# Kernel optimization log

Measured on AMD Instinct MI355X. Metric: run time of the kernel, lower is better.

## Reference

```python
import jax, jax.numpy as jnp
import numpy as np

NUM_REL = 5
NUM_BASES = 8
HID = 128
OUT = 64
IN_FEAT = 256
N_PER_TYPE = 50000
N_NODES = 2 * N_PER_TYPE
N_EDGES = 1000000
EPS = 1e-5  # PairNorm eps


def setup_inputs() -> dict:
    key = jax.random.key(0)
    ks = jax.random.split(key, 14)
    inp = {
        "x_author": jax.random.normal(ks[0], (N_PER_TYPE, IN_FEAT), jnp.float32),
        "x_paper": jax.random.normal(ks[1], (N_PER_TYPE, IN_FEAT), jnp.float32),
        "edge_index": jax.random.randint(ks[2], (2, N_EDGES), 0, N_NODES, jnp.int32),
        "edge_type": jax.random.randint(ks[3], (N_EDGES,), 0, NUM_REL, jnp.int32),
        # per-node-type input projections (nn.Linear)
        "proj_author_w": jax.random.normal(ks[4], (IN_FEAT, HID), jnp.float32) / np.sqrt(IN_FEAT),
        "proj_author_b": jnp.zeros((HID,), jnp.float32),
        "proj_paper_w": jax.random.normal(ks[5], (IN_FEAT, HID), jnp.float32) / np.sqrt(IN_FEAT),
        "proj_paper_b": jnp.zeros((HID,), jnp.float32),
        # RGCNConv layer 0 (hidden -> hidden), basis decomposition, root weight, no bias
        "comp0": jax.random.normal(ks[6], (NUM_REL, NUM_BASES), jnp.float32) / np.sqrt(NUM_BASES),
        "basis0": jax.random.normal(ks[7], (NUM_BASES, HID, HID), jnp.float32) / np.sqrt(HID),
        "root0": jax.random.normal(ks[8], (HID, HID), jnp.float32) / np.sqrt(HID),
        # RGCNConv layer 1 (hidden -> out)
        "comp1": jax.random.normal(ks[9], (NUM_REL, NUM_BASES), jnp.float32) / np.sqrt(NUM_BASES),
        "basis1": jax.random.normal(ks[10], (NUM_BASES, HID, OUT), jnp.float32) / np.sqrt(HID),
        "root1": jax.random.normal(ks[11], (HID, OUT), jnp.float32) / np.sqrt(HID),
    }
    return inp


def pairnorm(x):
    # PyG PairNorm (scale=1, scale_individually=False)
    x = x - x.mean(axis=0, keepdims=True)
    return x / jnp.sqrt(EPS + (x * x).sum(-1).mean())


def rgcn_conv(x, edge_index, edge_type, comp, basis, root):
    # weight[r] = sum_b comp[r,b] * basis[b]  -> [R, Fin, Fout]
    W = jnp.einsum('rb,bio->rio', comp, basis)
    src, dst = edge_index[0], edge_index[1]
    msgs = x[src]                                   # [E, Fin] gather
    seg = dst * NUM_REL + edge_type                 # per (node, relation) segment
    agg = jax.ops.segment_sum(msgs, seg, num_segments=N_NODES * NUM_REL)
    agg = agg.reshape(N_NODES, NUM_REL, -1)         # [N, R, Fin]
    cnt = jax.ops.segment_sum(jnp.ones((msgs.shape[0],), x.dtype), seg,
                              num_segments=N_NODES * NUM_REL).reshape(N_NODES, NUM_REL)
    mean = agg / jnp.maximum(cnt, 1.0)[..., None]   # mean aggregation (0 if no edges)
    return jnp.einsum('nrf,rfo->no', mean, W) + x @ root


def reference(x_author, x_paper, edge_index, edge_type,
              proj_author_w, proj_author_b, proj_paper_w, proj_paper_b,
              comp0, basis0, root0, comp1, basis1, root1):
    h_a = jax.nn.relu(x_author @ proj_author_w + proj_author_b)
    h_p = jax.nn.relu(x_paper @ proj_paper_w + proj_paper_b)
    x = jnp.concatenate([h_a, h_p], axis=0)         # [N, HID]
    x = jax.nn.relu(rgcn_conv(x, edge_index, edge_type, comp0, basis0, root0))
    x = pairnorm(x)
    x_latent = x
    x = rgcn_conv(x, edge_index, edge_type, comp1, basis1, root1)
    x = pairnorm(x)
    return (x, x_latent)
```

## Files before the change

kernel.cpp:

```cpp
#include <hip/hip_runtime.h>
#include <hip/hip_bf16.h>

constexpr int NPT    = 50000;
constexpr int NN     = 100000;
constexpr int NE     = 1000000;
constexpr int HID    = 128;
constexpr int OUTF   = 64;
constexpr int INF    = 256;
constexpr int NREL   = 5;
constexpr int NSEG   = NN * NREL;

typedef __attribute__((ext_vector_type(8))) short short8v;
typedef __attribute__((ext_vector_type(4))) float f32x4;

__device__ __forceinline__ ushort f2bf(float x) {
    uint u = __builtin_bit_cast(uint, x);
    uint r = (u + 0x7FFFu + ((u >> 16) & 1u)) >> 16;
    return (ushort)r;
}
__device__ __forceinline__ float bfhi(uint raw) {
    return __builtin_bit_cast(float, raw & 0xFFFF0000u);
}
__device__ __forceinline__ float bflo(uint raw) {
    return __builtin_bit_cast(float, raw << 16);
}

__device__ __forceinline__ void build_wbT_body(const float* __restrict__ comp,
                                               const float* __restrict__ basis,
                                               const float* __restrict__ root,
                                               ushort* __restrict__ wbT,
                                               int fout, int passOff, int idx) {
    int col = idx >> 7, k = idx & 127;
    float v;
    if (col < 320) {
        int r = col >> 6, f = (col & 63) + passOff;
        v = 0.f;
#pragma unroll
        for (int b = 0; b < 8; b++)
            v += comp[r * 8 + b] * basis[(b * 128 + k) * fout + f];
    } else {
        v = root[k * fout + (col - 320) + passOff];
    }
    wbT[col * 128 + k] = f2bf(v);
}

__global__ void prep_kernel(const float* __restrict__ comp0, const float* __restrict__ basis0,
                            const float* __restrict__ root0,
                            const float* __restrict__ comp1, const float* __restrict__ basis1,
                            const float* __restrict__ root1,
                            const float* __restrict__ paw, const float* __restrict__ ppw,
                            ushort* __restrict__ wbT0a, ushort* __restrict__ wbT0b,
                            ushort* __restrict__ wbT1,
                            ushort* __restrict__ wpa, ushort* __restrict__ wpp,
                            int* __restrict__ cnt, float* __restrict__ statscr,
                            int* __restrict__ recs_pad) {
    const int b = blockIdx.x, t = threadIdx.x;
    if (b < 1954) {
        int i = b * 256 + t;
        if (i < NSEG) cnt[i] = 0;
    } else if (b < 1979) {
        statscr[(b - 1954) * 256 + t] = 0.f;
    } else if (b == 1979) {
        if (t < 128) recs_pad[t] = 0;
    } else if (b < 2172) {
        build_wbT_body(comp0, basis0, root0, wbT0a, HID, 0, (b - 1980) * 256 + t);
    } else if (b < 2364) {
        build_wbT_body(comp0, basis0, root0, wbT0b, HID, 64, (b - 2172) * 256 + t);
    } else if (b < 2556) {
        build_wbT_body(comp1, basis1, root1, wbT1, OUTF, 0, (b - 2364) * 256 + t);
    } else if (b < 2684) {
        int i = (b - 2556) * 256 + t;
        wpa[(size_t)(i & 127) * 256 + (i >> 7)] = f2bf(paw[i]);
    } else {
        int i = (b - 2684) * 256 + t;
        wpp[(size_t)(i & 127) * 256 + (i >> 7)] = f2bf(ppw[i]);
    }
}

__launch_bounds__(256)
__global__ void proj_hist(const float* __restrict__ xa, const float* __restrict__ xp,
                          const ushort* __restrict__ wTa, const ushort* __restrict__ wTp,
                          const float* __restrict__ ba, const float* __restrict__ bp,
                          ushort* __restrict__ x0b,
                          const int* __restrict__ ei, const int* __restrict__ et,
                          int* __restrict__ cnt, int* __restrict__ rank) {
    __shared__ ushort sx[16][264];
    __shared__ ushort so[16][132];
    const int tid = threadIdx.x;
    if (blockIdx.x >= 1250) {
        int e = (blockIdx.x - 1250) * 256 + tid;
        if (e < NE) {
            int seg = ei[NE + e] * NREL + et[e];
            rank[e] = atomicAdd(&cnt[seg], 1);
        }
        return;
    }
    const bool author = blockIdx.x < 625;
    const int tile0 = (blockIdx.x - (author ? 0 : 625)) * 5;
    const float* x = author ? xa : xp;
    const ushort* wT = author ? wTa : wTp;
    const float* bias = author ? ba : bp;
    const int typeBase = author ? 0 : NPT;

    const int wave = tid >> 6, lane = tid & 63;
    const int row = lane & 15, g = lane >> 4;
    const int fcol = wave * 32 + row;

    const ushort* wp0 = wT + (size_t)fcol * 256 + g * 8;
    short8v bA[8], bB[8];
#pragma unroll
    for (int kk = 0; kk < 8; kk++) bA[kk] = *(const short8v*)&wp0[kk * 32];
#pragma unroll
    for (int kk = 0; kk < 8; kk++) bB[kk] = *(const short8v*)&wp0[16 * 256 + kk * 32];
    const float bv0 = bias[fcol], bv1 = bias[fcol + 16];

    const int sr = tid >> 4, part = tid & 15;
    const int fnode = tid >> 4, fb = (tid & 15) * 8;

    for (int t = 0; t < 5; t++) {
        const int nloc = (tile0 + t) * 16;
        {
            size_t rowoff = (size_t)(nloc + sr) * INF + part * 16;
#pragma unroll
            for (int ii = 0; ii < 4; ii++) {
                float4 v = *(const float4*)&x[rowoff + ii * 4];
                ushort4 h = {f2bf(v.x), f2bf(v.y), f2bf(v.z), f2bf(v.w)};
                *(ushort4*)&sx[sr][part * 16 + ii * 4] = h;
            }
        }
        __syncthreads();
        short8v a[8];
#pragma unroll
        for (int kk = 0; kk < 8; kk++) a[kk] = *(const short8v*)&sx[row][kk * 32 + g * 8];
        {
            f32x4 acc0 = {0.f, 0.f, 0.f, 0.f};
            f32x4 acc1 = {0.f, 0.f, 0.f, 0.f};
#pragma unroll
            for (int kk = 0; kk < 8; kk++) {
                acc0 = __builtin_amdgcn_mfma_f32_16x16x32_bf16(a[kk], bA[kk], acc0, 0, 0, 0);
                acc1 = __builtin_amdgcn_mfma_f32_16x16x32_bf16(a[kk], bB[kk], acc1, 0, 0, 0);
            }
#pragma unroll
            for (int q = 0; q < 4; q++) {
                so[g * 4 + q][fcol]      = f2bf(fmaxf(acc0[q] + bv0, 0.f));
                so[g * 4 + q][fcol + 16] = f2bf(fmaxf(acc1[q] + bv1, 0.f));
            }
        }
        __syncthreads();
        {
            ushort4 v0 = *(const ushort4*)&so[fnode][fb];
            ushort4 v1 = *(const ushort4*)&so[fnode][fb + 4];
            size_t gbase = (size_t)(typeBase + nloc + fnode) * 128 + fb;
            *(ushort4*)&x0b[gbase] = v0;
            *(ushort4*)&x0b[gbase + 4] = v1;
        }
    }
}

__global__ void scan1(const int* __restrict__ cnt, int* __restrict__ offs,
                      int* __restrict__ bsums, int n) {
    __shared__ int lds[256];
    const int t = threadIdx.x;
    const int base = blockIdx.x * 2048 + t * 8;
    int vals[8];
    int s = 0;
#pragma unroll
    for (int v = 0; v < 8; v++) {
        int idx = base + v;
        vals[v] = (idx < n) ? cnt[idx] : 0;
        s += vals[v];
    }
    lds[t] = s;
    __syncthreads();
    for (int off = 1; off < 256; off <<= 1) {
        int x = lds[t];
        int y = (t >= off) ? lds[t - off] : 0;
        __syncthreads();
        lds[t] = x + y;
        __syncthreads();
    }
    int run = (t > 0) ? lds[t - 1] : 0;
    if (t == 255) bsums[blockIdx.x] = lds[255];
#pragma unroll
    for (int v = 0; v < 8; v++) {
        int idx = base + v;
        if (idx < n) offs[idx] = run;
        run += vals[v];
    }
}

__global__ void scan2(const int* __restrict__ bsums, int* __restrict__ bsums2, int nb) {
    __shared__ int lds[256];
    const int t = threadIdx.x;
    lds[t] = (t < nb) ? bsums[t] : 0;
    __syncthreads();
    for (int off = 1; off < 256; off <<= 1) {
        int x = lds[t];
        int y = (t >= off) ? lds[t - off] : 0;
        __syncthreads();
        lds[t] = x + y;
        __syncthreads();
    }
    if (t < nb) bsums2[t] = (t > 0) ? lds[t - 1] : 0;
}

__global__ void scan3_desc(const int* __restrict__ offs, const int* __restrict__ bsums2,
                           const int* __restrict__ cnt, int2* __restrict__ desc, int n) {
    int i = blockIdx.x * blockDim.x + threadIdx.x;
    if (i < n) {
        int2 d = {offs[i] + bsums2[i >> 11], cnt[i]};
        desc[i] = d;
    }
}

__global__ void scatter_kernel(const int* __restrict__ ei, const int* __restrict__ et,
                               const int* __restrict__ rank,
                               const int2* __restrict__ desc, int2* __restrict__ recs) {
    int e = blockIdx.x * blockDim.x + threadIdx.x;
    if (e < NE) {
        int src = ei[e];
        int dst = ei[NE + e];
        int r = et[e];
        int2 d = desc[dst * NREL + r];
        int c = d.y;
        float sc = 1.f / (float)((c > 1) ? c : 1);
        int2 rec = {r * NN + src, __builtin_bit_cast(int, sc)};
        recs[d.x + rank[e]] = rec;
    }
}

__launch_bounds__(256)
__global__ void ytab_gemm0(const ushort* __restrict__ xin,
                           const ushort* __restrict__ wbT_a, const ushort* __restrict__ wbT_b,
                           ushort* __restrict__ ytab, float* __restrict__ hout) {
    __shared__ ushort sx[32][136];
    __shared__ ushort so[32][328];
    __shared__ float sroot[32][68];
    const int tid = threadIdx.x;
    const bool first = blockIdx.x < 625;
    const int tile0 = (first ? blockIdx.x : blockIdx.x - 625) * 5;
    const ushort* wbT = first ? wbT_a : wbT_b;
    const int outOff = first ? 0 : 64;
    const int wave = tid >> 6, lane = tid & 63;
    const int row = lane & 15, g = lane >> 4;
    const int wbase = wave * 96;

    const ushort* wp = wbT + (size_t)(wbase + row) * 128 + g * 8;
    short8v B[6][4];
#pragma unroll
    for (int t = 0; t < 6; t++)
#pragma unroll
        for (int kk = 0; kk < 4; kk++)
            B[t][kk] = *(const short8v*)&wp[t * 2048 + kk * 32];

    const int sr = tid >> 3, scl = (tid & 7) * 16;
    const int fnode = tid >> 3, fb = (tid & 7) * 8;

    for (int tt = 0; tt < 5; tt++) {
        const int n0 = (tile0 + tt) * 32;
        {
            const ushort* src = &xin[(size_t)(n0 + sr) * 128 + scl];
            *(short8v*)&sx[sr][scl] = *(const short8v*)&src[0];
            *(short8v*)&sx[sr][scl + 8] = *(const short8v*)&src[8];
        }
        __syncthreads();

        short8v a[2][4];
#pragma unroll
        for (int m = 0; m < 2; m++)
#pragma unroll
            for (int kk = 0; kk < 4; kk++)
                a[m][kk] = *(const short8v*)&sx[m * 16 + row][kk * 32 + g * 8];

#pragma unroll
        for (int t = 0; t < 6; t++) {
            f32x4 acc0 = {0.f, 0.f, 0.f, 0.f};
            f32x4 acc1 = {0.f, 0.f, 0.f, 0.f};
#pragma unroll
            for (int kk = 0; kk < 4; kk++) {
                acc0 = __builtin_amdgcn_mfma_f32_16x16x32_bf16(a[0][kk], B[t][kk], acc0, 0, 0, 0);
                acc1 = __builtin_amdgcn_mfma_f32_16x16x32_bf16(a[1][kk], B[t][kk], acc1, 0, 0, 0);
            }
            const int col = wbase + t * 16 + row;
            if (col < 320) {
#pragma unroll
                for (int q = 0; q < 4; q++) {
                    so[g * 4 + q][col] = f2bf(acc0[q]);
                    so[16 + g * 4 + q][col] = f2bf(acc1[q]);
                }
            } else {
                const int f = col - 320;
#pragma unroll
                for (int q = 0; q < 4; q++) {
                    sroot[g * 4 + q][f] = acc0[q];
                    sroot[16 + g * 4 + q][f] = acc1[q];
                }
            }
        }
        __syncthreads();

        {
#pragma unroll
            for (int r = 0; r < NREL; r++) {
                short8v v = *(const short8v*)&so[fnode][r * 64 + fb];
                *(short8v*)&ytab[(size_t)r * NN * 128 + (size_t)(n0 + fnode) * 128
                                 + outOff + fb] = v;
            }
            float4 r0 = *(const float4*)&sroot[fnode][fb];
            float4 r1 = *(const float4*)&sroot[fnode][fb + 4];
            float* hp = &hout[(size_t)(n0 + fnode) * HID + outOff + fb];
            *(float4*)&hp[0] = r0;
            *(float4*)&hp[4] = r1;
        }
    }
}

__launch_bounds__(256)
__global__ void ytab_gemm1(float* __restrict__ h0x, const float* __restrict__ mu,
                           const ushort* __restrict__ wbT,
                           ushort* __restrict__ ytab, float* __restrict__ h1) {
    __shared__ ushort sx[32][136];
    __shared__ ushort so[32][328];
    __shared__ float sroot[32][68];
    const int tid = threadIdx.x;
    const int tile0 = blockIdx.x * 5;
    const int wave = tid >> 6, lane = tid & 63;
    const int row = lane & 15, g = lane >> 4;
    const int wbase = wave * 96;

    const ushort* wp = wbT + (size_t)(wbase + row) * 128 + g * 8;
    short8v B[6][4];
#pragma unroll
    for (int t = 0; t < 6; t++)
#pragma unroll
        for (int kk = 0; kk < 4; kk++)
            B[t][kk] = *(const short8v*)&wp[t * 2048 + kk * 32];

    const int sr = tid >> 3, scl = (tid & 7) * 16;
    const int fnode = tid >> 3, fb = (tid & 7) * 8;

    float m[16];
#pragma unroll
    for (int i = 0; i < 16; i++) m[i] = mu[scl + i];
    const float s = mu[128];

    for (int tt = 0; tt < 5; tt++) {
        const int n0 = (tile0 + tt) * 32;
        {
            float* hp = &h0x[(size_t)(n0 + sr) * 128 + scl];
            float v[16];
#pragma unroll
            for (int i = 0; i < 4; i++) {
                float4 t4 = *(const float4*)&hp[i * 4];
                v[i * 4 + 0] = (t4.x - m[i * 4 + 0]) * s;
                v[i * 4 + 1] = (t4.y - m[i * 4 + 1]) * s;
                v[i * 4 + 2] = (t4.z - m[i * 4 + 2]) * s;
                v[i * 4 + 3] = (t4.w - m[i * 4 + 3]) * s;
            }
            ushort hb[16];
#pragma unroll
            for (int i = 0; i < 16; i++) hb[i] = f2bf(v[i]);
#pragma unroll
            for (int i = 0; i < 4; i++) {
                float4 t4 = {v[i * 4], v[i * 4 + 1], v[i * 4 + 2], v[i * 4 + 3]};
                *(float4*)&hp[i * 4] = t4;
            }
            *(short8v*)&sx[sr][scl] = *(const short8v*)&hb[0];
            *(short8v*)&sx[sr][scl + 8] = *(const short8v*)&hb[8];
        }
        __syncthreads();

        short8v a[2][4];
#pragma unroll
        for (int mi = 0; mi < 2; mi++)
#pragma unroll
            for (int kk = 0; kk < 4; kk++)
                a[mi][kk] = *(const short8v*)&sx[mi * 16 + row][kk * 32 + g * 8];

#pragma unroll
        for (int t = 0; t < 6; t++) {
            f32x4 acc0 = {0.f, 0.f, 0.f, 0.f};
            f32x4 acc1 = {0.f, 0.f, 0.f, 0.f};
#pragma unroll
            for (int kk = 0; kk < 4; kk++) {
                acc0 = __builtin_amdgcn_mfma_f32_16x16x32_bf16(a[0][kk], B[t][kk], acc0, 0, 0, 0);
                acc1 = __builtin_amdgcn_mfma_f32_16x16x32_bf16(a[1][kk], B[t][kk], acc1, 0, 0, 0);
            }
            const int col = wbase + t * 16 + row;
            if (col < 320) {
#pragma unroll
                for (int q = 0; q < 4; q++) {
                    so[g * 4 + q][col] = f2bf(acc0[q]);
                    so[16 + g * 4 + q][col] = f2bf(acc1[q]);
                }
            } else {
                const int f = col - 320;
#pragma unroll
                for (int q = 0; q < 4; q++) {
                    sroot[g * 4 + q][f] = acc0[q];
                    sroot[16 + g * 4 + q][f] = acc1[q];
                }
            }
        }
        __syncthreads();

        {
#pragma unroll
            for (int r = 0; r < NREL; r++) {
                short8v v = *(const short8v*)&so[fnode][r * 64 + fb];
                *(short8v*)&ytab[(size_t)r * NN * 64 + (size_t)(n0 + fnode) * 64 + fb] = v;
            }
            float4 r0 = *(const float4*)&sroot[fnode][fb];
            float4 r1 = *(const float4*)&sroot[fnode][fb + 4];
            float* hp = &h1[(size_t)(n0 + fnode) * OUTF + fb];
            *(float4*)&hp[0] = r0;
            *(float4*)&hp[4] = r1;
        }
    }
}

template <int FW, bool RELU>
__launch_bounds__(256)
__global__ void agg_kernel(const ushort* __restrict__ ytab,
                           const int2* __restrict__ recs,
                           const int2* __restrict__ desc,
                           float* __restrict__ hout,
                           float* __restrict__ csrep, float* __restrict__ ssrep) {
    constexpr int FPL = FW / 32;
    __shared__ float sred[4][32][FPL + 1];
    const int tid = threadIdx.x;
    const int wave = tid >> 6, lane = tid & 63;
    const int half = lane >> 5, fl = lane & 31;
    const int n0 = blockIdx.x * 16 + wave * 4;

    int start[4], total[4];
#pragma unroll
    for (int rep = 0; rep < 4; rep++) {
        const int s5 = (n0 + rep) * NREL;
        int2 d0 = desc[s5];
        int2 d4 = desc[s5 + 4];
        start[rep] = d0.x;
        total[rep] = d4.x + d4.y - d0.x;
    }
    int2 rec[4];
#pragma unroll
    for (int rep = 0; rep < 4; rep++) {
        rec[rep].x = 0; rec[rep].y = 0;
        if (lane < total[rep]) rec[rep] = recs[start[rep] + lane];
    }

    float hpre[4][FPL];
#pragma unroll
    for (int rep = 0; rep < 4; rep++) {
        const float* hp = &hout[(size_t)(n0 + rep) * FW + fl * FPL];
#pragma unroll
        for (int q = 0; q < FPL; q++) hpre[rep][q] = hp[q];
    }

    float cs_loc[FPL];
#pragma unroll
    for (int q = 0; q < FPL; q++) cs_loc[q] = 0.f;
    float ss_loc = 0.f;

#pragma unroll
    for (int rep = 0; rep < 4; rep++) {
        float acc[FPL];
#pragma unroll
        for (int q = 0; q < FPL; q++) acc[q] = 0.f;
        const int lim = (total[rep] > 64) ? 64 : total[rep];
#pragma unroll 2
        for (int j2 = half; j2 < lim; j2 += 2) {
            int rw = __shfl(rec[rep].x, j2);
            float sc = __builtin_bit_cast(float, __shfl(rec[rep].y, j2));
            if (FW == 128) {
                uint2 raw = *(const uint2*)&ytab[(size_t)rw * FW + fl * 4];
                acc[0] += sc * bflo(raw.x);
                acc[1] += sc * bfhi(raw.x);
                acc[2] += sc * bflo(raw.y);
                acc[3] += sc * bfhi(raw.y);
            } else {
                uint raw = *(const uint*)&ytab[(size_t)rw * FW + fl * 2];
                acc[0] += sc * bflo(raw);
                acc[1] += sc * bfhi(raw);
            }
        }
        if (total[rep] > 64) {
            for (int j = 64 + half; j < total[rep]; j += 2) {
                int2 r2 = recs[start[rep] + j];
                float sc = __builtin_bit_cast(float, r2.y);
                if (FW == 128) {
                    uint2 raw = *(const uint2*)&ytab[(size_t)r2.x * FW + fl * 4];
                    acc[0] += sc * bflo(raw.x);
                    acc[1] += sc * bfhi(raw.x);
                    acc[2] += sc * bflo(raw.y);
                    acc[3] += sc * bfhi(raw.y);
                } else {
                    uint raw = *(const uint*)&ytab[(size_t)r2.x * FW + fl * 2];
                    acc[0] += sc * bflo(raw);
                    acc[1] += sc * bfhi(raw);
                }
            }
        }
#pragma unroll
        for (int q = 0; q < FPL; q++) acc[q] += __shfl_xor(acc[q], 32);
        if (half == 0) {
            float o[FPL];
#pragma unroll
            for (int q = 0; q < FPL; q++) {
                o[q] = hpre[rep][q] + acc[q];
                if (RELU) o[q] = fmaxf(o[q], 0.f);
                cs_loc[q] += o[q];
                ss_loc += o[q] * o[q];
            }
            float* hp = &hout[(size_t)(n0 + rep) * FW + fl * FPL];
            if (FW == 128) *(float4*)hp = *(float4*)o;
            else           *(float2*)hp = *(float2*)o;
        }
    }

    if (half == 0) {
#pragma unroll
        for (int q = 0; q < FPL; q++) sred[wave][fl][q] = cs_loc[q];
        sred[wave][fl][FPL] = ss_loc;
    }
    __syncthreads();
    if (tid < 32) {
        float sq[FPL + 1];
#pragma unroll
        for (int q = 0; q <= FPL; q++)
            sq[q] = sred[0][tid][q] + sred[1][tid][q] + sred[2][tid][q] + sred[3][tid][q];
        const int repl = blockIdx.x & 31;
#pragma unroll
        for (int q = 0; q < FPL; q++)
            atomicAdd(&csrep[repl * FW + tid * FPL + q], sq[q]);
        float ssv = sq[FPL];
#pragma unroll
        for (int mof = 16; mof > 0; mof >>= 1) ssv += __shfl_xor(ssv, mof);
        if (tid == 0) atomicAdd(&ssrep[repl], ssv);
    }
}

template <int F>
__global__ void finalize_rep(const float* __restrict__ csrep,
                             const float* __restrict__ ssrep,
                             float* __restrict__ mu_inv) {
    __shared__ float sred[128];
    const int f = threadIdx.x;
    float s = 0.f;
    for (int r = 0; r < 32; r++) s += csrep[r * F + f];
    float mu = s / (float)NN;
    mu_inv[f] = mu;
    sred[f] = mu * mu;
    __syncthreads();
    for (int h = F / 2; h > 0; h >>= 1) {
        if (f < h) sred[f] += sred[f + h];
        __syncthreads();
    }
    if (f == 0) {
        float ss = 0.f;
        for (int r = 0; r < 32; r++) ss += ssrep[r];
        float var = ss / (float)NN - sred[0];
        mu_inv[F] = rsqrtf(1e-5f + var);
    }
}

template <int F>
__global__ void normalize_kernel(const float* __restrict__ x,
                                 const float* __restrict__ mu_inv,
                                 float* __restrict__ out, int total4) {
    int i = blockIdx.x * blockDim.x + threadIdx.x;
    if (i < total4) {
        int base = i * 4;
        int f = base & (F - 1);
        float4 v = *(const float4*)&x[base];
        float4 m = *(const float4*)&mu_inv[f];
        float s = mu_inv[F];
        float4 o = {(v.x - m.x) * s, (v.y - m.y) * s, (v.z - m.z) * s, (v.w - m.w) * s};
        *(float4*)&out[base] = o;
    }
}

extern "C" void kernel_launch(void* const* d_in, const int* in_sizes, int n_in,
                              void* d_out, int out_size, void* d_ws, size_t ws_size,
                              hipStream_t stream) {
    const float* xa    = (const float*)d_in[0];
    const float* xp    = (const float*)d_in[1];
    const int*   ei    = (const int*)d_in[2];
    const int*   et    = (const int*)d_in[3];
    const float* paw   = (const float*)d_in[4];
    const float* pab   = (const float*)d_in[5];
    const float* ppw   = (const float*)d_in[6];
    const float* ppb   = (const float*)d_in[7];
    const float* comp0 = (const float*)d_in[8];
    const float* basis0= (const float*)d_in[9];
    const float* root0 = (const float*)d_in[10];
    const float* comp1 = (const float*)d_in[11];
    const float* basis1= (const float*)d_in[12];
    const float* root1 = (const float*)d_in[13];
    float* out = (float*)d_out;

    char* ws = (char*)d_ws;
    size_t o = 0;
    auto alloc = [&](size_t b) { size_t p = o; o += (b + 255) & ~(size_t)255; return p; };
    ushort* x0b    = (ushort*)(ws + alloc((size_t)NN * HID * 2));
    ushort* ytab   = (ushort*)(ws + alloc((size_t)NREL * NN * 128 * 2));
    int2*   desc   = (int2*)(ws + alloc((size_t)NSEG * 8));
    int2*   recs   = (int2*)(ws + alloc((size_t)(NE + 64) * 8));
    ushort* wbT0a  = (ushort*)(ws + alloc(384 * 128 * 2));
    ushort* wbT0b  = (ushort*)(ws + alloc(384 * 128 * 2));
    ushort* wbT1   = (ushort*)(ws + alloc(384 * 128 * 2));
    ushort* wpa    = (ushort*)(ws + alloc(128 * 256 * 2));
    ushort* wpp    = (ushort*)(ws + alloc(128 * 256 * 2));
    float*  statscr= (float*)(ws + alloc(6400 * 4));
    float*  mu0    = (float*)(ws + alloc(129 * 4));
    float*  mu1    = (float*)(ws + alloc(65 * 4));
    float* cs0rep = statscr;
    float* ss0rep = statscr + 4096;
    float* cs1rep = statscr + 4128;
    float* ss1rep = statscr + 6176;

    char* ybase = (char*)ytab;
    int* cnt    = (int*)(ybase);
    int* offs   = (int*)(ybase + (size_t)NSEG * 4);
    int* rank   = (int*)(ybase + (size_t)NSEG * 8);
    int* bsums  = (int*)(ybase + (size_t)NSEG * 8 + (size_t)NE * 4);
    int* bsums2 = (int*)(ybase + (size_t)NSEG * 8 + (size_t)NE * 4 + 4096);

    float* h0 = out + (size_t)NN * OUTF;
    float* h1 = out;

    prep_kernel<<<2812, 256, 0, stream>>>(comp0, basis0, root0, comp1, basis1, root1,
                                          paw, ppw, wbT0a, wbT0b, wbT1, wpa, wpp,
                                          cnt, statscr, (int*)(recs + NE));
    proj_hist<<<1250 + (NE + 255) / 256, 256, 0, stream>>>(xa, xp, wpa, wpp, pab, ppb,
                                                           x0b, ei, et, cnt, rank);

    const int nb = (NSEG + 2047) / 2048;
    scan1<<<nb, 256, 0, stream>>>(cnt, offs, bsums, NSEG);
    scan2<<<1, 256, 0, stream>>>(bsums, bsums2, nb);
    scan3_desc<<<(NSEG + 255) / 256, 256, 0, stream>>>(offs, bsums2, cnt, desc, NSEG);
    scatter_kernel<<<(NE + 255) / 256, 256, 0, stream>>>(ei, et, rank, desc, recs);

    ytab_gemm0<<<1250, 256, 0, stream>>>(x0b, wbT0a, wbT0b, ytab, h0);
    agg_kernel<128, true><<<NN / 16, 256, 0, stream>>>(ytab, recs, desc, h0, cs0rep, ss0rep);
    finalize_rep<128><<<1, 128, 0, stream>>>(cs0rep, ss0rep, mu0);

    ytab_gemm1<<<625, 256, 0, stream>>>(h0, mu0, wbT1, ytab, h1);
    agg_kernel<64, false><<<NN / 16, 256, 0, stream>>>(ytab, recs, desc, h1, cs1rep, ss1rep);
    finalize_rep<64><<<1, 64, 0, stream>>>(cs1rep, ss1rep, mu1);
    normalize_kernel<OUTF><<<(NN * OUTF / 4 + 255) / 256, 256, 0, stream>>>(h1, mu1, out,
                                                                            NN * OUTF / 4);
}
```

Measured before the change: 364.3 us.

## Fuse edge scatter into layer-0 GEMM launch and widen aggregation gathers

Merges the edge scatter kernel into the layer-0 ytab GEMM launch as extra blocks. This removes one launch and lets the scatter overlap with the GEMM; the rank buffer moves out of the ytab region so the two no longer alias. The aggregation kernel now has 4 edge slots per wave with 16 lanes per row, so each lane loads 16 or 8 bytes instead of 8 or 4, with a two-step shuffle reduction. Record loads are no longer masked by lane count, so padding past the end of the record array is relied on.

```diff
diff --git a/kernel.cpp b/kernel.cpp
--- a/kernel.cpp
+++ b/kernel.cpp
@@ -213,30 +213,31 @@
     }
 }
 
-__global__ void scatter_kernel(const int* __restrict__ ei, const int* __restrict__ et,
-                               const int* __restrict__ rank,
-                               const int2* __restrict__ desc, int2* __restrict__ recs) {
-    int e = blockIdx.x * blockDim.x + threadIdx.x;
-    if (e < NE) {
-        int src = ei[e];
-        int dst = ei[NE + e];
-        int r = et[e];
-        int2 d = desc[dst * NREL + r];
-        int c = d.y;
-        float sc = 1.f / (float)((c > 1) ? c : 1);
-        int2 rec = {r * NN + src, __builtin_bit_cast(int, sc)};
-        recs[d.x + rank[e]] = rec;
-    }
-}
-
 __launch_bounds__(256)
-__global__ void ytab_gemm0(const ushort* __restrict__ xin,
-                           const ushort* __restrict__ wbT_a, const ushort* __restrict__ wbT_b,
-                           ushort* __restrict__ ytab, float* __restrict__ hout) {
+__global__ void gemm0_scatter(const ushort* __restrict__ xin,
+                              const ushort* __restrict__ wbT_a, const ushort* __restrict__ wbT_b,
+                              ushort* __restrict__ ytab, float* __restrict__ hout,
+                              const int* __restrict__ ei, const int* __restrict__ et,
+                              const int* __restrict__ rank,
+                              const int2* __restrict__ desc, int2* __restrict__ recs) {
     __shared__ ushort sx[32][136];
     __shared__ ushort so[32][328];
     __shared__ float sroot[32][68];
     const int tid = threadIdx.x;
+    if (blockIdx.x >= 1250) {
+        int e = (blockIdx.x - 1250) * 256 + tid;
+        if (e < NE) {
+            int src = ei[e];
+            int dst = ei[NE + e];
+            int r = et[e];
+            int2 d = desc[dst * NREL + r];
+            int c = d.y;
+            float sc = 1.f / (float)((c > 1) ? c : 1);
+            int2 rec = {r * NN + src, __builtin_bit_cast(int, sc)};
+            recs[d.x + rank[e]] = rec;
+        }
+        return;
+    }
     const bool first = blockIdx.x < 625;
     const int tile0 = (first ? blockIdx.x : blockIdx.x - 625) * 5;
     const ushort* wbT = first ? wbT_a : wbT_b;
@@ -426,11 +427,11 @@
                            const int2* __restrict__ desc,
                            float* __restrict__ hout,
                            float* __restrict__ csrep, float* __restrict__ ssrep) {
-    constexpr int FPL = FW / 32;
-    __shared__ float sred[4][32][FPL + 1];
+    constexpr int FPL = FW / 16;
+    __shared__ float sred[4][16][FPL + 1];
     const int tid = threadIdx.x;
     const int wave = tid >> 6, lane = tid & 63;
-    const int half = lane >> 5, fl = lane & 31;
+    const int q = lane >> 4, fl = lane & 15;
     const int n0 = blockIdx.x * 16 + wave * 4;
 
     int start[4], total[4];
@@ -442,100 +443,104 @@
         start[rep] = d0.x;
         total[rep] = d4.x + d4.y - d0.x;
     }
-    int2 rec[4];
-#pragma unroll
-    for (int rep = 0; rep < 4; rep++) {
-        rec[rep].x = 0; rec[rep].y = 0;
-        if (lane < total[rep]) rec[rep] = recs[start[rep] + lane];
-    }
-
     float hpre[4][FPL];
 #pragma unroll
     for (int rep = 0; rep < 4; rep++) {
         const float* hp = &hout[(size_t)(n0 + rep) * FW + fl * FPL];
 #pragma unroll
-        for (int q = 0; q < FPL; q++) hpre[rep][q] = hp[q];
-    }
+        for (int k = 0; k < FPL; k++) hpre[rep][k] = hp[k];
+    }
+    int2 rec[4];
+#pragma unroll
+    for (int rep = 0; rep < 4; rep++) rec[rep] = recs[start[rep] + lane];
 
     float cs_loc[FPL];
 #pragma unroll
-    for (int q = 0; q < FPL; q++) cs_loc[q] = 0.f;
+    for (int k = 0; k < FPL; k++) cs_loc[k] = 0.f;
     float ss_loc = 0.f;
 
 #pragma unroll
     for (int rep = 0; rep < 4; rep++) {
         float acc[FPL];
 #pragma unroll
-        for (int q = 0; q < FPL; q++) acc[q] = 0.f;
+        for (int k = 0; k < FPL; k++) acc[k] = 0.f;
         const int lim = (total[rep] > 64) ? 64 : total[rep];
+        const int iters = (lim + 3) >> 2;
 #pragma unroll 2
-        for (int j2 = half; j2 < lim; j2 += 2) {
-            int rw = __shfl(rec[rep].x, j2);
-            float sc = __builtin_bit_cast(float, __shfl(rec[rep].y, j2));
+        for (int it = 0; it < iters; it++) {
+            const int j4 = it * 4 + q;
+            int rwr = __shfl(rec[rep].x, j4);
+            int scb = __shfl(rec[rep].y, j4);
+            const bool ok = j4 < lim;
+            const int rw = ok ? rwr : 0;
+            const float sc = ok ? __builtin_bit_cast(float, scb) : 0.f;
             if (FW == 128) {
+                uint4 raw = *(const uint4*)&ytab[(size_t)rw * FW + fl * 8];
+                acc[0] += sc * bflo(raw.x); acc[1] += sc * bfhi(raw.x);
+                acc[2] += sc * bflo(raw.y); acc[3] += sc * bfhi(raw.y);
+                acc[4] += sc * bflo(raw.z); acc[5] += sc * bfhi(raw.z);
+                acc[6] += sc * bflo(raw.w); acc[7] += sc * bfhi(raw.w);
+            } else {
                 uint2 raw = *(const uint2*)&ytab[(size_t)rw * FW + fl * 4];
-                acc[0] += sc * bflo(raw.x);
-                acc[1] += sc * bfhi(raw.x);
-                acc[2] += sc * bflo(raw.y);
-                acc[3] += sc * bfhi(raw.y);
-            } else {
-                uint raw = *(const uint*)&ytab[(size_t)rw * FW + fl * 2];
-                acc[0] += sc * bflo(raw);
-                acc[1] += sc * bfhi(raw);
+                acc[0] += sc * bflo(raw.x); acc[1] += sc * bfhi(raw.x);
+                acc[2] += sc * bflo(raw.y); acc[3] += sc * bfhi(raw.y);
             }
         }
         if (total[rep] > 64) {
-            for (int j = 64 + half; j < total[rep]; j += 2) {
+            for (int j = 64 + q; j < total[rep]; j += 4) {
                 int2 r2 = recs[start[rep] + j];
                 float sc = __builtin_bit_cast(float, r2.y);
                 if (FW == 128) {
+                    uint4 raw = *(const uint4*)&ytab[(size_t)r2.x * FW + fl * 8];
+                    acc[0] += sc * bflo(raw.x); acc[1] += sc * bfhi(raw.x);
+                    acc[2] += sc * bflo(raw.y); acc[3] += sc * bfhi(raw.y);
+                    acc[4] += sc * bflo(raw.z); acc[5] += sc * bfhi(raw.z);
+                    acc[6] += sc * bflo(raw.w); acc[7] += sc * bfhi(raw.w);
+                } else {
                     uint2 raw = *(const uint2*)&ytab[(size_t)r2.x * FW + fl * 4];
-                    acc[0] += sc * bflo(raw.x);
-                    acc[1] += sc * bfhi(raw.x);
-                    acc[2] += sc * bflo(raw.y);
-                    acc[3] += sc * bfhi(raw.y);
-                } else {
-                    uint raw = *(const uint*)&ytab[(size_t)r2.x * FW + fl * 2];
-                    acc[0] += sc * bflo(raw);
-                    acc[1] += sc * bfhi(raw);
+                    acc[0] += sc * bflo(raw.x); acc[1] += sc * bfhi(raw.x);
+                    acc[2] += sc * bflo(raw.y); acc[3] += sc * bfhi(raw.y);
                 }
             }
         }
 #pragma unroll
-        for (int q = 0; q < FPL; q++) acc[q] += __shfl_xor(acc[q], 32);
-        if (half == 0) {
+        for (int k = 0; k < FPL; k++) {
+            acc[k] += __shfl_xor(acc[k], 32);
+            acc[k] += __shfl_xor(acc[k], 16);
+        }
+        if (q == 0) {
             float o[FPL];
 #pragma unroll
-            for (int q = 0; q < FPL; q++) {
-                o[q] = hpre[rep][q] + acc[q];
-                if (RELU) o[q] = fmaxf(o[q], 0.f);
-                cs_loc[q] += o[q];
-                ss_loc += o[q] * o[q];
+            for (int k = 0; k < FPL; k++) {
+                o[k] = hpre[rep][k] + acc[k];
+                if (RELU) o[k] = fmaxf(o[k], 0.f);
+                cs_loc[k] += o[k];
+                ss_loc += o[k] * o[k];
             }
             float* hp = &hout[(size_t)(n0 + rep) * FW + fl * FPL];
-            if (FW == 128) *(float4*)hp = *(float4*)o;
-            else           *(float2*)hp = *(float2*)o;
-        }
-    }
-
-    if (half == 0) {
-#pragma unroll
-        for (int q = 0; q < FPL; q++) sred[wave][fl][q] = cs_loc[q];
+#pragma unroll
+            for (int k = 0; k < FPL; k += 4)
+                *(float4*)&hp[k] = *(float4*)&o[k];
+        }
+    }
+
+    if (q == 0) {
+#pragma unroll
+        for (int k = 0; k < FPL; k++) sred[wave][fl][k] = cs_loc[k];
         sred[wave][fl][FPL] = ss_loc;
     }
     __syncthreads();
-    if (tid < 32) {
-        float sq[FPL + 1];
-#pragma unroll
-        for (int q = 0; q <= FPL; q++)
-            sq[q] = sred[0][tid][q] + sred[1][tid][q] + sred[2][tid][q] + sred[3][tid][q];
-        const int repl = blockIdx.x & 31;
-#pragma unroll
-        for (int q = 0; q < FPL; q++)
-            atomicAdd(&csrep[repl * FW + tid * FPL + q], sq[q]);
-        float ssv = sq[FPL];
-#pragma unroll
-        for (int mof = 16; mof > 0; mof >>= 1) ssv += __shfl_xor(ssv, mof);
+    const int repl = blockIdx.x & 31;
+    if (tid < FW) {
+        int k = tid & (FPL - 1), f2 = tid / FPL;
+        float sv = sred[0][f2][k] + sred[1][f2][k] + sred[2][f2][k] + sred[3][f2][k];
+        atomicAdd(&csrep[repl * FW + f2 * FPL + k], sv);
+    }
+    if (tid < 16) {
+        float ssv = sred[0][tid][FPL] + sred[1][tid][FPL]
+                  + sred[2][tid][FPL] + sred[3][tid][FPL];
+#pragma unroll
+        for (int mof = 8; mof > 0; mof >>= 1) ssv += __shfl_xor(ssv, mof);
         if (tid == 0) atomicAdd(&ssrep[repl], ssv);
     }
 }
@@ -606,6 +611,7 @@
     ushort* ytab   = (ushort*)(ws + alloc((size_t)NREL * NN * 128 * 2));
     int2*   desc   = (int2*)(ws + alloc((size_t)NSEG * 8));
     int2*   recs   = (int2*)(ws + alloc((size_t)(NE + 64) * 8));
+    int*    rank   = (int*)(ws + alloc((size_t)NE * 4));
     ushort* wbT0a  = (ushort*)(ws + alloc(384 * 128 * 2));
     ushort* wbT0b  = (ushort*)(ws + alloc(384 * 128 * 2));
     ushort* wbT1   = (ushort*)(ws + alloc(384 * 128 * 2));
@@ -622,9 +628,8 @@
     char* ybase = (char*)ytab;
     int* cnt    = (int*)(ybase);
     int* offs   = (int*)(ybase + (size_t)NSEG * 4);
-    int* rank   = (int*)(ybase + (size_t)NSEG * 8);
-    int* bsums  = (int*)(ybase + (size_t)NSEG * 8 + (size_t)NE * 4);
-    int* bsums2 = (int*)(ybase + (size_t)NSEG * 8 + (size_t)NE * 4 + 4096);
+    int* bsums  = (int*)(ybase + (size_t)NSEG * 8);
+    int* bsums2 = (int*)(ybase + (size_t)NSEG * 8 + 4096);
 
     float* h0 = out + (size_t)NN * OUTF;
     float* h1 = out;
@@ -639,9 +644,9 @@
     scan1<<<nb, 256, 0, stream>>>(cnt, offs, bsums, NSEG);
     scan2<<<1, 256, 0, stream>>>(bsums, bsums2, nb);
     scan3_desc<<<(NSEG + 255) / 256, 256, 0, stream>>>(offs, bsums2, cnt, desc, NSEG);
-    scatter_kernel<<<(NE + 255) / 256, 256, 0, stream>>>(ei, et, rank, desc, recs);
-
-    ytab_gemm0<<<1250, 256, 0, stream>>>(x0b, wbT0a, wbT0b, ytab, h0);
+
+    gemm0_scatter<<<1250 + (NE + 255) / 256, 256, 0, stream>>>(
+        x0b, wbT0a, wbT0b, ytab, h0, ei, et, rank, desc, recs);
     agg_kernel<128, true><<<NN / 16, 256, 0, stream>>>(ytab, recs, desc, h0, cs0rep, ss0rep);
     finalize_rep<128><<<1, 128, 0, stream>>>(cs0rep, ss0rep, mu0);
 
```

After: 345.5 us. -5.2%, faster.
